# Optimization experiments

Hardware: AMD Instinct MI355X
Metric: run time of the kernel (lower is better)

The kernel has to match this reference:

```python
import jax, jax.numpy as jnp
import numpy as np

B, NQ, NK, D = 8, 2048, 2048, 512

def setup_inputs() -> dict:
    key = jax.random.key(0)
    ks = jax.random.split(key, 6)
    s = 1.0 / np.sqrt(D)
    return {
        "query": jax.random.normal(ks[0], (B, NQ, D), dtype=jnp.float32),
        "key":   jax.random.normal(ks[1], (B, NK, D), dtype=jnp.float32),
        "value": jax.random.normal(ks[2], (B, NK, D), dtype=jnp.float32),
        "Wq": jax.random.normal(ks[3], (D, D), dtype=jnp.float32) * s,
        "Wk": jax.random.normal(ks[4], (D, D), dtype=jnp.float32) * s,
        "Wv": jax.random.normal(ks[5], (D, D), dtype=jnp.float32) * s,
    }

def reference(query, key, value, Wq, Wk, Wv):
    # nn.Linear(bias=False): y = x @ W.T
    q = jnp.einsum('bnd,ed->bne', query, Wq)
    k = jnp.einsum('bnd,ed->bne', key, Wk)
    v = jnp.einsum('bnd,ed->bne', value, Wv)
    # NOTE: original module applies NO 1/sqrt(d) scaling
    scores = jnp.einsum('bqd,bkd->bqk', q, k)   # [B, NQ, NK]
    weights = jax.nn.softmax(scores, axis=-1)
    return jnp.einsum('bqk,bkd->bqd', weights, v)
```

## Files before the change

### kernel.cpp

```cpp
#include <hip/hip_runtime.h>

typedef __attribute__((ext_vector_type(8))) short short8;
typedef __attribute__((ext_vector_type(8))) _Float16 half8;
typedef __attribute__((ext_vector_type(4))) float f32x4;
typedef __attribute__((ext_vector_type(4))) unsigned short u16x4;
typedef __attribute__((ext_vector_type(4))) _Float16 half4;

#define NB 8
#define NQL 2048
#define NKL 2048
#define DD 512

static __device__ __forceinline__ void stage16(const void* g, void* l){
  __builtin_amdgcn_global_load_lds(
      (const __attribute__((address_space(1))) void*)g,
      (__attribute__((address_space(3))) void*)l, 16, 0, 0);
}

static __device__ __forceinline__ void barrier_lgkm(){
  asm volatile("s_waitcnt lgkmcnt(0)" ::: "memory");
  __builtin_amdgcn_s_barrier();
  asm volatile("" ::: "memory");
}

__global__ __launch_bounds__(256) void split3_k(
    const float* __restrict__ Wq, const float* __restrict__ Wk, const float* __restrict__ Wv,
    _Float16* __restrict__ w16q, _Float16* __restrict__ w16k, _Float16* __restrict__ w16v,
    int n4){
  const int z = blockIdx.y;
  const float* x = (z==0) ? Wq : (z==1) ? Wk : Wv;
  _Float16* o16 = (z==0) ? w16q : (z==1) ? w16k : w16v;
  int i = blockIdx.x*256 + threadIdx.x;
  if (i >= n4) return;
  f32x4 v = reinterpret_cast<const f32x4*>(x)[i];
  half4 h;
  #pragma unroll
  for (int j=0;j<4;j++) h[j] = (_Float16)v[j];
  reinterpret_cast<half4*>(o16)[i] = h;
}

__global__ __launch_bounds__(256, 2) void proj2_k(
    const float* __restrict__ Xq, const float* __restrict__ Xk, const float* __restrict__ Xv,
    const _Float16* __restrict__ W16q, const _Float16* __restrict__ W16k, const _Float16* __restrict__ W16v,
    _Float16* __restrict__ Yq,
    _Float16* __restrict__ Ykt,
    _Float16* __restrict__ Yvt)
{
  __shared__ _Float16 AB[2][2][128][32];

  const int z = blockIdx.z;
  const float*    X  = (z==0) ? Xq   : (z==1) ? Xk   : Xv;
  const _Float16* Wf = (z==0) ? W16q : (z==1) ? W16k : W16v;

  const int mbase = blockIdx.x * 128;
  const int nbase = blockIdx.y * 128;
  const int tid = threadIdx.x;
  const int w = tid >> 6, lane = tid & 63;
  const int l15 = lane & 15, l4 = lane >> 4;
  const int wr = w >> 1, wc = w & 1;

  const int arow = tid >> 1, ahalf = tid & 1;
  const int brow_l = w*16 + (lane>>2);
  const int bkg    = (lane & 3) ^ ((lane >> 3) & 3);

  f32x4 acc[4][4];
  #pragma unroll
  for (int m=0;m<4;m++)
    #pragma unroll
    for (int n=0;n<4;n++) acc[m][n] = (f32x4){0.f,0.f,0.f,0.f};

  f32x4 xa[4];
  {
    const f32x4* xp = reinterpret_cast<const f32x4*>(X + (size_t)(mbase+arow)*DD + ahalf*16);
    #pragma unroll
    for (int q=0;q<4;q++) xa[q] = xp[q];
  }
  {
    _Float16* lB = &AB[0][1][0][0] + w*512;
    #pragma unroll
    for (int r=0;r<2;r++){
      const size_t gh = (size_t)(nbase + r*64 + brow_l)*DD + bkg*8;
      stage16(Wf + gh, lB + r*2048);
    }
  }
  {
    asm volatile("s_waitcnt vmcnt(2)" ::: "memory");
    half8 a0, a1;
    #pragma unroll
    for (int j=0;j<4;j++){
      a0[j] = (_Float16)xa[0][j]; a0[4+j] = (_Float16)xa[1][j];
      a1[j] = (_Float16)xa[2][j]; a1[4+j] = (_Float16)xa[3][j];
    }
    const int sw = (arow>>1)&3;
    const int cg0 = (ahalf*2) ^ sw, cg1 = (ahalf*2+1) ^ sw;
    *reinterpret_cast<half8*>(&AB[0][0][arow][cg0*8]) = a0;
    *reinterpret_cast<half8*>(&AB[0][0][arow][cg1*8]) = a1;
  }

  const int asw = (l15>>1)&3;

  #pragma unroll 1
  for (int s=0; s<16; ++s){
    const int cur = s&1, nxt = cur^1;
    asm volatile("s_waitcnt vmcnt(0)" ::: "memory");
    barrier_lgkm();

    if (s < 15){
      const f32x4* xp = reinterpret_cast<const f32x4*>(X + (size_t)(mbase+arow)*DD + (s+1)*32 + ahalf*16);
      #pragma unroll
      for (int q=0;q<4;q++) xa[q] = xp[q];
      _Float16* lB = &AB[nxt][1][0][0] + w*512;
      #pragma unroll
      for (int r=0;r<2;r++){
        const size_t gh = (size_t)(nbase + r*64 + brow_l)*DD + (s+1)*32 + bkg*8;
        stage16(Wf + gh, lB + r*2048);
      }
    }

    half8 ah[4], wf[4];
    #pragma unroll
    for (int m=0;m<4;m++){
      const int rA = wr*64 + m*16 + l15;
      const int cg = (l4 ^ asw)*8;
      ah[m] = *reinterpret_cast<const half8*>(&AB[cur][0][rA][cg]);
    }
    #pragma unroll
    for (int n=0;n<4;n++){
      const int rB = wc*64 + n*16 + l15;
      const int cg = (l4 ^ asw)*8;
      wf[n] = *reinterpret_cast<const half8*>(&AB[cur][1][rB][cg]);
    }
    #pragma unroll
    for (int m=0;m<4;m++)
      #pragma unroll
      for (int n=0;n<4;n++) acc[m][n] = __builtin_amdgcn_mfma_f32_16x16x32_f16(ah[m], wf[n], acc[m][n], 0,0,0);

    if (s < 15){
      asm volatile("s_waitcnt vmcnt(2)" ::: "memory");
      half8 a0, a1;
      #pragma unroll
      for (int j=0;j<4;j++){
        a0[j] = (_Float16)xa[0][j]; a0[4+j] = (_Float16)xa[1][j];
        a1[j] = (_Float16)xa[2][j]; a1[4+j] = (_Float16)xa[3][j];
      }
      const int sw = (arow>>1)&3;
      const int cg0 = (ahalf*2) ^ sw, cg1 = (ahalf*2+1) ^ sw;
      *reinterpret_cast<half8*>(&AB[nxt][0][arow][cg0*8]) = a0;
      *reinterpret_cast<half8*>(&AB[nxt][0][arow][cg1*8]) = a1;
    }
  }

  #pragma unroll
  for (int m=0;m<4;m++){
    #pragma unroll
    for (int n=0;n<4;n++){
      #pragma unroll
      for (int j=0;j<4;j++){
        const int row = mbase + wr*64 + m*16 + l4*4 + j;
        const int col = nbase + wc*64 + n*16 + l15;
        const float y = acc[m][n][j];
        if (z == 0){
          Yq[(size_t)row*DD + col] = (_Float16)y;
        } else if (z == 1){
          const int bb = row >> 11, nn = row & 2047, kt = nn >> 5;
          const size_t tb = ((size_t)(bb*64 + kt)) << 14;
          const int kr = nn & 31, cg = col >> 3, ci = col & 7;
          const size_t idx = tb + ((size_t)kr)*512 + (size_t)((((cg ^ (kr & 7)) << 3)) | ci);
          Ykt[idx] = (_Float16)y;
        } else {
          const int bb = row >> 11, nn = row & 2047, kt = nn >> 5;
          const size_t tb = ((size_t)(bb*64 + kt)) << 14;
          const int kk = nn & 31;
          const size_t idx = tb + ((size_t)col)*32 + (size_t)kk;
          Yvt[idx] = (_Float16)y;
        }
      }
    }
  }
}

__global__ __launch_bounds__(256, 2) void attn_k(
    const _Float16* __restrict__ Qf,
    const _Float16* __restrict__ Kt,
    const _Float16* __restrict__ Vt,
    float* __restrict__ Out)
{
  __shared__ _Float16 K_lds[2][32][512];
  __shared__ _Float16 P_s[2][32][40];
  __shared__ float sc_s[2][32];
  __shared__ float l_s[32];

  const int bid = blockIdx.x;
  const int b  = bid & 7;
  const int qt = bid >> 3;
  const int tid = threadIdx.x;
  const int w = tid >> 6, lane = tid & 63;
  const int l15 = lane & 15, l4 = lane >> 4;
  const bool isQK = (w < 2);
  const int qw = w & 1;

  const _Float16* gK = Kt + ((size_t)(b*64) << 14);
  const _Float16* gV = Vt + ((size_t)(b*64) << 14);
  const int goff  = w*512 + lane*8;
  const int lbase = w*512;

  f32x4 r[32];
  half8 vr[16];
  float m_old = -1e30f, lacc = 0.f;
  if (isQK){
    const size_t qoff = (size_t)(b*NQL + qt*32 + qw*16 + l15)*DD + l4*8;
    #pragma unroll
    for (int kc=0;kc<16;kc++){
      r[kc] = __builtin_bit_cast(f32x4, *reinterpret_cast<const half8*>(Qf + qoff + kc*32));
    }
  } else {
    #pragma unroll
    for (int i=0;i<32;i++) r[i] = (f32x4){0.f,0.f,0.f,0.f};
  }

  {
    _Float16* lK = &K_lds[0][0][0];
    #pragma unroll
    for (int q=0;q<8;q++) stage16(gK + q*2048 + goff, lK + q*2048 + lbase);
  }

  const int kx = l15 & 7;
  const int row_i = qw*16 + l15;
  const int vcol = qw*256 + l15;

  #pragma unroll 1
  for (int kt=0; kt<64; ++kt){
    const int par = kt & 1;
    asm volatile("s_waitcnt vmcnt(0)" ::: "memory");
    barrier_lgkm();

    if (kt < 63){
      const _Float16* g = gK + ((size_t)(kt+1) << 14);
      _Float16* lK = &K_lds[par^1][0][0];
      #pragma unroll
      for (int q=0;q<8;q++) stage16(g + q*2048 + goff, lK + q*2048 + lbase);
    }

    if (isQK){
      f32x4 s0 = (f32x4){0.f,0.f,0.f,0.f};
      f32x4 s1 = (f32x4){0.f,0.f,0.f,0.f};
      __builtin_amdgcn_s_setprio(1);
      #pragma unroll
      for (int kc=0;kc<16;kc++){
        const int cg = ((kc*4 + l4) ^ kx) << 3;
        const half8 kf0 = *reinterpret_cast<const half8*>(&K_lds[par][l15][cg]);
        const half8 kf1 = *reinterpret_cast<const half8*>(&K_lds[par][16+l15][cg]);
        const half8 q = __builtin_bit_cast(half8, r[kc]);
        s0 = __builtin_amdgcn_mfma_f32_16x16x32_f16(kf0, q, s0, 0,0,0);
        s1 = __builtin_amdgcn_mfma_f32_16x16x32_f16(kf1, q, s1, 0,0,0);
      }
      __builtin_amdgcn_s_setprio(0);
      const f32x4 sv0 = s0;
      const f32x4 sv1 = s1;

      float mw = fmaxf(fmaxf(fmaxf(sv0[0],sv0[1]), fmaxf(sv0[2],sv0[3])),
                       fmaxf(fmaxf(sv1[0],sv1[1]), fmaxf(sv1[2],sv1[3])));
      float p0 = __expf(sv0[0]-m_old), p1 = __expf(sv0[1]-m_old);
      float p2 = __expf(sv0[2]-m_old), p3 = __expf(sv0[3]-m_old);
      float p4 = __expf(sv1[0]-m_old), p5 = __expf(sv1[1]-m_old);
      float p6 = __expf(sv1[2]-m_old), p7 = __expf(sv1[3]-m_old);
      mw = fmaxf(mw, __shfl_xor(mw, 16));
      mw = fmaxf(mw, __shfl_xor(mw, 32));
      float e_old = 1.0f;
      if (mw > m_old + 8.0f){
        e_old = __expf(m_old - mw);
        p0 = __expf(sv0[0]-mw); p1 = __expf(sv0[1]-mw);
        p2 = __expf(sv0[2]-mw); p3 = __expf(sv0[3]-mw);
        p4 = __expf(sv1[0]-mw); p5 = __expf(sv1[1]-mw);
        p6 = __expf(sv1[2]-mw); p7 = __expf(sv1[3]-mw);
        m_old = mw;
      }
      if (l4 == 0) sc_s[par][row_i] = e_old;
      uint2 hv;
      hv.x = (unsigned)__builtin_bit_cast(unsigned short,(_Float16)p0) |
             ((unsigned)__builtin_bit_cast(unsigned short,(_Float16)p1)<<16);
      hv.y = (unsigned)__builtin_bit_cast(unsigned short,(_Float16)p2) |
             ((unsigned)__builtin_bit_cast(unsigned short,(_Float16)p3)<<16);
      *reinterpret_cast<uint2*>(&P_s[par][row_i][l4*4]) = hv;
      uint2 hw;
      hw.x = (unsigned)__builtin_bit_cast(unsigned short,(_Float16)p4) |
             ((unsigned)__builtin_bit_cast(unsigned short,(_Float16)p5)<<16);
      hw.y = (unsigned)__builtin_bit_cast(unsigned short,(_Float16)p6) |
             ((unsigned)__builtin_bit_cast(unsigned short,(_Float16)p7)<<16);
      *reinterpret_cast<uint2*>(&P_s[par][row_i][16 + l4*4]) = hw;
      float ssum = (p0+p1)+(p2+p3)+((p4+p5)+(p6+p7));
      ssum += __shfl_xor(ssum, 16);
      ssum += __shfl_xor(ssum, 32);
      lacc = lacc*e_old + ssum;
    } else {
      const int pp = par^1;
      if (kt > 0){
        float scs[2][4];
        bool need = false;
        #pragma unroll
        for (int rg=0;rg<2;rg++)
          #pragma unroll
          for (int j=0;j<4;j++){
            scs[rg][j] = sc_s[pp][rg*16 + l4*4 + j];
            need = need || (scs[rg][j] < 0.999999f);
          }
        if (__any(need)){
          #pragma unroll
          for (int rg=0;rg<2;rg++)
            #pragma unroll
            for (int f=0;f<16;f++)
              #pragma unroll
              for (int j=0;j<4;j++) r[rg*16+f][j] *= scs[rg][j];
        }
        const half8 pa0 = *reinterpret_cast<const half8*>(&P_s[pp][l15][l4*8]);
        const half8 pa1 = *reinterpret_cast<const half8*>(&P_s[pp][16+l15][l4*8]);
        __builtin_amdgcn_s_setprio(1);
        #pragma unroll
        for (int f=0;f<16;f++){
          r[f]    = __builtin_amdgcn_mfma_f32_16x16x32_f16(pa0, vr[f], r[f],    0,0,0);
          r[16+f] = __builtin_amdgcn_mfma_f32_16x16x32_f16(pa1, vr[f], r[16+f], 0,0,0);
        }
        __builtin_amdgcn_s_setprio(0);
      }
      {
        const _Float16* g = gV + ((size_t)kt << 14);
        #pragma unroll
        for (int f=0;f<16;f++){
          vr[f] = *reinterpret_cast<const half8*>(g + (size_t)(vcol + f*16)*32 + l4*8);
        }
      }
    }
  }

  if (isQK && l4 == 0) l_s[row_i] = lacc;
  asm volatile("s_waitcnt vmcnt(0)" ::: "memory");
  barrier_lgkm();

  if (!isQK){
    float scs[2][4];
    bool need = false;
    #pragma unroll
    for (int rg=0;rg<2;rg++)
      #pragma unroll
      for (int j=0;j<4;j++){
        scs[rg][j] = sc_s[1][rg*16 + l4*4 + j];
        need = need || (scs[rg][j] < 0.999999f);
      }
    if (__any(need)){
      #pragma unroll
      for (int rg=0;rg<2;rg++)
        #pragma unroll
        for (int f=0;f<16;f++)
          #pragma unroll
          for (int j=0;j<4;j++) r[rg*16+f][j] *= scs[rg][j];
    }
    const half8 pa0 = *reinterpret_cast<const half8*>(&P_s[1][l15][l4*8]);
    const half8 pa1 = *reinterpret_cast<const half8*>(&P_s[1][16+l15][l4*8]);
    #pragma unroll
    for (int f=0;f<16;f++){
      r[f]    = __builtin_amdgcn_mfma_f32_16x16x32_f16(pa0, vr[f], r[f],    0,0,0);
      r[16+f] = __builtin_amdgcn_mfma_f32_16x16x32_f16(pa1, vr[f], r[16+f], 0,0,0);
    }
    float inv[2][4];
    #pragma unroll
    for (int rg=0;rg<2;rg++)
      #pragma unroll
      for (int j=0;j<4;j++) inv[rg][j] = 1.0f / l_s[rg*16 + l4*4 + j];
    #pragma unroll
    for (int rg=0;rg<2;rg++){
      #pragma unroll
      for (int j=0;j<4;j++){
        const int row = rg*16 + l4*4 + j;
        const size_t obase = (size_t)(b*NQL + qt*32 + row)*DD;
        #pragma unroll
        for (int f=0;f<16;f++){
          Out[obase + qw*256 + f*16 + l15] = r[rg*16+f][j]*inv[rg][j];
        }
      }
    }
  }
}

extern "C" void kernel_launch(void* const* d_in, const int* in_sizes, int n_in,
                              void* d_out, int out_size, void* d_ws, size_t ws_size,
                              hipStream_t stream) {
  const float* query = (const float*)d_in[0];
  const float* key   = (const float*)d_in[1];
  const float* value = (const float*)d_in[2];
  const float* Wq    = (const float*)d_in[3];
  const float* Wk    = (const float*)d_in[4];
  const float* Wv    = (const float*)d_in[5];
  float* out = (float*)d_out;

  const size_t SB = (size_t)NB*NQL*DD;
  const size_t WB = (size_t)DD*DD;

  _Float16* p = (_Float16*)d_ws;
  _Float16 *w16q = p, *w16k = p + WB, *w16v = p + 2*WB;
  _Float16* q0 = p + 3*WB;
  _Float16 *q16  = q0;
  _Float16 *Kt16 = q0 + SB;
  _Float16 *Vt16 = q0 + 2*SB;

  dim3 sg(256, 3);
  split3_k<<<sg, 256, 0, stream>>>(Wq, Wk, Wv, w16q, w16k, w16v, (int)(WB/4));

  dim3 pg(128, 4, 3);
  proj2_k<<<pg, 256, 0, stream>>>(query, key, value,
                                  w16q, w16k, w16v,
                                  q16, Kt16, Vt16);

  attn_k<<<512, 256, 0, stream>>>(q16, Kt16, Vt16, out);
}
```

Baseline: 173.8 us.

## Double attention tile to 64 queries and 64 keys with 512-thread blocks

The attention kernel now processes 64 query rows and 64-key tiles per block, using 8 waves (4 for QK/softmax, 4 for PV). The K/V projection output layout changes to 64-key tiles to match. This halves the number of K-tile iterations and barriers, and halves total K/V traffic per query. The cost is larger LDS use (about 130KB), fewer blocks (256, so one per CU), and a different PV register tiling.

```diff
diff --git a/kernel.cpp b/kernel.cpp
--- a/kernel.cpp
+++ b/kernel.cpp
@@ -162,16 +162,16 @@
         if (z == 0){
           Yq[(size_t)row*DD + col] = (_Float16)y;
         } else if (z == 1){
-          const int bb = row >> 11, nn = row & 2047, kt = nn >> 5;
-          const size_t tb = ((size_t)(bb*64 + kt)) << 14;
-          const int kr = nn & 31, cg = col >> 3, ci = col & 7;
+          const int bb = row >> 11, nn = row & 2047, kt = nn >> 6;
+          const size_t tb = ((size_t)(bb*32 + kt)) << 15;
+          const int kr = nn & 63, cg = col >> 3, ci = col & 7;
           const size_t idx = tb + ((size_t)kr)*512 + (size_t)((((cg ^ (kr & 7)) << 3)) | ci);
           Ykt[idx] = (_Float16)y;
         } else {
-          const int bb = row >> 11, nn = row & 2047, kt = nn >> 5;
-          const size_t tb = ((size_t)(bb*64 + kt)) << 14;
-          const int kk = nn & 31;
-          const size_t idx = tb + ((size_t)col)*32 + (size_t)kk;
+          const int bb = row >> 11, nn = row & 2047, kt = nn >> 6;
+          const size_t tb = ((size_t)(bb*32 + kt)) << 15;
+          const int kk = nn & 63;
+          const size_t idx = tb + ((size_t)col)*64 + (size_t)kk;
           Yvt[idx] = (_Float16)y;
         }
       }
@@ -179,16 +179,16 @@
   }
 }
 
-__global__ __launch_bounds__(256, 2) void attn_k(
+__global__ __launch_bounds__(512, 2) void attn_k(
     const _Float16* __restrict__ Qf,
     const _Float16* __restrict__ Kt,
     const _Float16* __restrict__ Vt,
     float* __restrict__ Out)
 {
-  __shared__ _Float16 K_lds[2][32][512];
-  __shared__ _Float16 P_s[2][32][40];
-  __shared__ float sc_s[2][32];
-  __shared__ float l_s[32];
+  __shared__ _Float16 K_lds[2][64][512];
+  __shared__ _Float16 P_s[2][64][72];
+  __shared__ float sc_s[2][64];
+  __shared__ float l_s[64];
 
   const int bid = blockIdx.x;
   const int b  = bid & 7;
@@ -196,11 +196,11 @@
   const int tid = threadIdx.x;
   const int w = tid >> 6, lane = tid & 63;
   const int l15 = lane & 15, l4 = lane >> 4;
-  const bool isQK = (w < 2);
-  const int qw = w & 1;
-
-  const _Float16* gK = Kt + ((size_t)(b*64) << 14);
-  const _Float16* gV = Vt + ((size_t)(b*64) << 14);
+  const bool isQK = (w < 4);
+  const int qw = w & 3;
+
+  const _Float16* gK = Kt + ((size_t)(b*32) << 15);
+  const _Float16* gV = Vt + ((size_t)(b*32) << 15);
   const int goff  = w*512 + lane*8;
   const int lbase = w*512;
 
@@ -208,7 +208,7 @@
   half8 vr[16];
   float m_old = -1e30f, lacc = 0.f;
   if (isQK){
-    const size_t qoff = (size_t)(b*NQL + qt*32 + qw*16 + l15)*DD + l4*8;
+    const size_t qoff = (size_t)(b*NQL + qt*64 + qw*16 + l15)*DD + l4*8;
     #pragma unroll
     for (int kc=0;kc<16;kc++){
       r[kc] = __builtin_bit_cast(f32x4, *reinterpret_cast<const half8*>(Qf + qoff + kc*32));
@@ -221,113 +221,140 @@
   {
     _Float16* lK = &K_lds[0][0][0];
     #pragma unroll
-    for (int q=0;q<8;q++) stage16(gK + q*2048 + goff, lK + q*2048 + lbase);
+    for (int q=0;q<8;q++) stage16(gK + q*4096 + goff, lK + q*4096 + lbase);
   }
 
   const int kx = l15 & 7;
   const int row_i = qw*16 + l15;
-  const int vcol = qw*256 + l15;
 
   #pragma unroll 1
-  for (int kt=0; kt<64; ++kt){
+  for (int kt=0; kt<32; ++kt){
     const int par = kt & 1;
     asm volatile("s_waitcnt vmcnt(0)" ::: "memory");
     barrier_lgkm();
 
-    if (kt < 63){
-      const _Float16* g = gK + ((size_t)(kt+1) << 14);
+    if (kt < 31){
+      const _Float16* g = gK + ((size_t)(kt+1) << 15);
       _Float16* lK = &K_lds[par^1][0][0];
       #pragma unroll
-      for (int q=0;q<8;q++) stage16(g + q*2048 + goff, lK + q*2048 + lbase);
+      for (int q=0;q<8;q++) stage16(g + q*4096 + goff, lK + q*4096 + lbase);
     }
 
     if (isQK){
       f32x4 s0 = (f32x4){0.f,0.f,0.f,0.f};
       f32x4 s1 = (f32x4){0.f,0.f,0.f,0.f};
+      f32x4 s2 = (f32x4){0.f,0.f,0.f,0.f};
+      f32x4 s3 = (f32x4){0.f,0.f,0.f,0.f};
       __builtin_amdgcn_s_setprio(1);
       #pragma unroll
       for (int kc=0;kc<16;kc++){
         const int cg = ((kc*4 + l4) ^ kx) << 3;
         const half8 kf0 = *reinterpret_cast<const half8*>(&K_lds[par][l15][cg]);
         const half8 kf1 = *reinterpret_cast<const half8*>(&K_lds[par][16+l15][cg]);
+        const half8 kf2 = *reinterpret_cast<const half8*>(&K_lds[par][32+l15][cg]);
+        const half8 kf3 = *reinterpret_cast<const half8*>(&K_lds[par][48+l15][cg]);
         const half8 q = __builtin_bit_cast(half8, r[kc]);
         s0 = __builtin_amdgcn_mfma_f32_16x16x32_f16(kf0, q, s0, 0,0,0);
         s1 = __builtin_amdgcn_mfma_f32_16x16x32_f16(kf1, q, s1, 0,0,0);
+        s2 = __builtin_amdgcn_mfma_f32_16x16x32_f16(kf2, q, s2, 0,0,0);
+        s3 = __builtin_amdgcn_mfma_f32_16x16x32_f16(kf3, q, s3, 0,0,0);
       }
       __builtin_amdgcn_s_setprio(0);
-      const f32x4 sv0 = s0;
-      const f32x4 sv1 = s1;
-
-      float mw = fmaxf(fmaxf(fmaxf(sv0[0],sv0[1]), fmaxf(sv0[2],sv0[3])),
-                       fmaxf(fmaxf(sv1[0],sv1[1]), fmaxf(sv1[2],sv1[3])));
-      float p0 = __expf(sv0[0]-m_old), p1 = __expf(sv0[1]-m_old);
-      float p2 = __expf(sv0[2]-m_old), p3 = __expf(sv0[3]-m_old);
-      float p4 = __expf(sv1[0]-m_old), p5 = __expf(sv1[1]-m_old);
-      float p6 = __expf(sv1[2]-m_old), p7 = __expf(sv1[3]-m_old);
+
+      float mw = fmaxf(fmaxf(fmaxf(s0[0],s0[1]), fmaxf(s0[2],s0[3])),
+                       fmaxf(fmaxf(s1[0],s1[1]), fmaxf(s1[2],s1[3])));
+      mw = fmaxf(mw, fmaxf(fmaxf(fmaxf(s2[0],s2[1]), fmaxf(s2[2],s2[3])),
+                           fmaxf(fmaxf(s3[0],s3[1]), fmaxf(s3[2],s3[3]))));
+      float p0[4], p1[4], p2[4], p3[4];
+      #pragma unroll
+      for (int j=0;j<4;j++){
+        p0[j] = __expf(s0[j]-m_old); p1[j] = __expf(s1[j]-m_old);
+        p2[j] = __expf(s2[j]-m_old); p3[j] = __expf(s3[j]-m_old);
+      }
       mw = fmaxf(mw, __shfl_xor(mw, 16));
       mw = fmaxf(mw, __shfl_xor(mw, 32));
       float e_old = 1.0f;
       if (mw > m_old + 8.0f){
         e_old = __expf(m_old - mw);
-        p0 = __expf(sv0[0]-mw); p1 = __expf(sv0[1]-mw);
-        p2 = __expf(sv0[2]-mw); p3 = __expf(sv0[3]-mw);
-        p4 = __expf(sv1[0]-mw); p5 = __expf(sv1[1]-mw);
-        p6 = __expf(sv1[2]-mw); p7 = __expf(sv1[3]-mw);
+        #pragma unroll
+        for (int j=0;j<4;j++){
+          p0[j] = __expf(s0[j]-mw); p1[j] = __expf(s1[j]-mw);
+          p2[j] = __expf(s2[j]-mw); p3[j] = __expf(s3[j]-mw);
+        }
         m_old = mw;
       }
       if (l4 == 0) sc_s[par][row_i] = e_old;
       uint2 hv;
-      hv.x = (unsigned)__builtin_bit_cast(unsigned short,(_Float16)p0) |
-             ((unsigned)__builtin_bit_cast(unsigned short,(_Float16)p1)<<16);
-      hv.y = (unsigned)__builtin_bit_cast(unsigned short,(_Float16)p2) |
-             ((unsigned)__builtin_bit_cast(unsigned short,(_Float16)p3)<<16);
+      hv.x = (unsigned)__builtin_bit_cast(unsigned short,(_Float16)p0[0]) |
+             ((unsigned)__builtin_bit_cast(unsigned short,(_Float16)p0[1])<<16);
+      hv.y = (unsigned)__builtin_bit_cast(unsigned short,(_Float16)p0[2]) |
+             ((unsigned)__builtin_bit_cast(unsigned short,(_Float16)p0[3])<<16);
       *reinterpret_cast<uint2*>(&P_s[par][row_i][l4*4]) = hv;
-      uint2 hw;
-      hw.x = (unsigned)__builtin_bit_cast(unsigned short,(_Float16)p4) |
-             ((unsigned)__builtin_bit_cast(unsigned short,(_Float16)p5)<<16);
-      hw.y = (unsigned)__builtin_bit_cast(unsigned short,(_Float16)p6) |
-             ((unsigned)__builtin_bit_cast(unsigned short,(_Float16)p7)<<16);
-      *reinterpret_cast<uint2*>(&P_s[par][row_i][16 + l4*4]) = hw;
-      float ssum = (p0+p1)+(p2+p3)+((p4+p5)+(p6+p7));
+      hv.x = (unsigned)__builtin_bit_cast(unsigned short,(_Float16)p1[0]) |
+             ((unsigned)__builtin_bit_cast(unsigned short,(_Float16)p1[1])<<16);
+      hv.y = (unsigned)__builtin_bit_cast(unsigned short,(_Float16)p1[2]) |
+             ((unsigned)__builtin_bit_cast(unsigned short,(_Float16)p1[3])<<16);
+      *reinterpret_cast<uint2*>(&P_s[par][row_i][16 + l4*4]) = hv;
+      hv.x = (unsigned)__builtin_bit_cast(unsigned short,(_Float16)p2[0]) |
+             ((unsigned)__builtin_bit_cast(unsigned short,(_Float16)p2[1])<<16);
+      hv.y = (unsigned)__builtin_bit_cast(unsigned short,(_Float16)p2[2]) |
+             ((unsigned)__builtin_bit_cast(unsigned short,(_Float16)p2[3])<<16);
+      *reinterpret_cast<uint2*>(&P_s[par][row_i][32 + l4*4]) = hv;
+      hv.x = (unsigned)__builtin_bit_cast(unsigned short,(_Float16)p3[0]) |
+             ((unsigned)__builtin_bit_cast(unsigned short,(_Float16)p3[1])<<16);
+      hv.y = (unsigned)__builtin_bit_cast(unsigned short,(_Float16)p3[2]) |
+             ((unsigned)__builtin_bit_cast(unsigned short,(_Float16)p3[3])<<16);
+      *reinterpret_cast<uint2*>(&P_s[par][row_i][48 + l4*4]) = hv;
+      float ssum = (p0[0]+p0[1])+(p0[2]+p0[3]) + (p1[0]+p1[1])+(p1[2]+p1[3])
+                 + (p2[0]+p2[1])+(p2[2]+p2[3]) + (p3[0]+p3[1])+(p3[2]+p3[3]);
       ssum += __shfl_xor(ssum, 16);
       ssum += __shfl_xor(ssum, 32);
       lacc = lacc*e_old + ssum;
     } else {
       const int pp = par^1;
       if (kt > 0){
-        float scs[2][4];
+        float scs[4][4];
         bool need = false;
         #pragma unroll
-        for (int rg=0;rg<2;rg++)
+        for (int rf=0;rf<4;rf++)
           #pragma unroll
           for (int j=0;j<4;j++){
-            scs[rg][j] = sc_s[pp][rg*16 + l4*4 + j];
-            need = need || (scs[rg][j] < 0.999999f);
+            scs[rf][j] = sc_s[pp][rf*16 + l4*4 + j];
+            need = need || (scs[rf][j] < 0.999999f);
           }
         if (__any(need)){
           #pragma unroll
-          for (int rg=0;rg<2;rg++)
+          for (int rf=0;rf<4;rf++)
             #pragma unroll
-            for (int f=0;f<16;f++)
+            for (int cf=0;cf<8;cf++)
               #pragma unroll
-              for (int j=0;j<4;j++) r[rg*16+f][j] *= scs[rg][j];
+              for (int j=0;j<4;j++) r[rf*8+cf][j] *= scs[rf][j];
         }
-        const half8 pa0 = *reinterpret_cast<const half8*>(&P_s[pp][l15][l4*8]);
-        const half8 pa1 = *reinterpret_cast<const half8*>(&P_s[pp][16+l15][l4*8]);
+        half8 pa[4][2];
+        #pragma unroll
+        for (int rf=0;rf<4;rf++)
+          #pragma unroll
+          for (int kc=0;kc<2;kc++)
+            pa[rf][kc] = *reinterpret_cast<const half8*>(&P_s[pp][rf*16 + l15][kc*32 + l4*8]);
         __builtin_amdgcn_s_setprio(1);
         #pragma unroll
-        for (int f=0;f<16;f++){
-          r[f]    = __builtin_amdgcn_mfma_f32_16x16x32_f16(pa0, vr[f], r[f],    0,0,0);
-          r[16+f] = __builtin_amdgcn_mfma_f32_16x16x32_f16(pa1, vr[f], r[16+f], 0,0,0);
-        }
+        for (int rf=0;rf<4;rf++)
+          #pragma unroll
+          for (int cf=0;cf<8;cf++){
+            r[rf*8+cf] = __builtin_amdgcn_mfma_f32_16x16x32_f16(pa[rf][0], vr[cf],   r[rf*8+cf], 0,0,0);
+            r[rf*8+cf] = __builtin_amdgcn_mfma_f32_16x16x32_f16(pa[rf][1], vr[8+cf], r[rf*8+cf], 0,0,0);
+          }
         __builtin_amdgcn_s_setprio(0);
       }
       {
-        const _Float16* g = gV + ((size_t)kt << 14);
-        #pragma unroll
-        for (int f=0;f<16;f++){
-          vr[f] = *reinterpret_cast<const half8*>(g + (size_t)(vcol + f*16)*32 + l4*8);
-        }
+        const _Float16* g = gV + ((size_t)kt << 15);
+        #pragma unroll
+        for (int kc=0;kc<2;kc++)
+          #pragma unroll
+          for (int cf=0;cf<8;cf++){
+            const int dcol = qw*128 + cf*16 + l15;
+            vr[kc*8+cf] = *reinterpret_cast<const half8*>(g + (size_t)dcol*64 + kc*32 + l4*8);
+          }
       }
     }
   }
@@ -337,44 +364,48 @@
   barrier_lgkm();
 
   if (!isQK){
-    float scs[2][4];
+    float scs[4][4];
     bool need = false;
     #pragma unroll
-    for (int rg=0;rg<2;rg++)
+    for (int rf=0;rf<4;rf++)
       #pragma unroll
       for (int j=0;j<4;j++){
-        scs[rg][j] = sc_s[1][rg*16 + l4*4 + j];
-        need = need || (scs[rg][j] < 0.999999f);
+        scs[rf][j] = sc_s[1][rf*16 + l4*4 + j];
+        need = need || (scs[rf][j] < 0.999999f);
       }
     if (__any(need)){
       #pragma unroll
-      for (int rg=0;rg<2;rg++)
-        #pragma unroll
-        for (int f=0;f<16;f++)
-          #pragma unroll
-          for (int j=0;j<4;j++) r[rg*16+f][j] *= scs[rg][j];
-    }
-    const half8 pa0 = *reinterpret_cast<const half8*>(&P_s[1][l15][l4*8]);
-    const half8 pa1 = *reinterpret_cast<const half8*>(&P_s[1][16+l15][l4*8]);
-    #pragma unroll
-    for (int f=0;f<16;f++){
-      r[f]    = __builtin_amdgcn_mfma_f32_16x16x32_f16(pa0, vr[f], r[f],    0,0,0);
-      r[16+f] = __builtin_amdgcn_mfma_f32_16x16x32_f16(pa1, vr[f], r[16+f], 0,0,0);
-    }
-    float inv[2][4];
-    #pragma unroll
-    for (int rg=0;rg<2;rg++)
-      #pragma unroll
-      for (int j=0;j<4;j++) inv[rg][j] = 1.0f / l_s[rg*16 + l4*4 + j];
-    #pragma unroll
-    for (int rg=0;rg<2;rg++){
+      for (int rf=0;rf<4;rf++)
+        #pragma unroll
+        for (int cf=0;cf<8;cf++)
+          #pragma unroll
+          for (int j=0;j<4;j++) r[rf*8+cf][j] *= scs[rf][j];
+    }
+    half8 pa[4][2];
+    #pragma unroll
+    for (int rf=0;rf<4;rf++)
+      #pragma unroll
+      for (int kc=0;kc<2;kc++)
+        pa[rf][kc] = *reinterpret_cast<const half8*>(&P_s[1][rf*16 + l15][kc*32 + l4*8]);
+    #pragma unroll
+    for (int rf=0;rf<4;rf++)
+      #pragma unroll
+      for (int cf=0;cf<8;cf++){
+        r[rf*8+cf] = __builtin_amdgcn_mfma_f32_16x16x32_f16(pa[rf][0], vr[cf],   r[rf*8+cf], 0,0,0);
+        r[rf*8+cf] = __builtin_amdgcn_mfma_f32_16x16x32_f16(pa[rf][1], vr[8+cf], r[rf*8+cf], 0,0,0);
+      }
+    #pragma unroll
+    for (int rf=0;rf<4;rf++){
+      float inv[4];
+      #pragma unroll
+      for (int j=0;j<4;j++) inv[j] = 1.0f / l_s[rf*16 + l4*4 + j];
       #pragma unroll
       for (int j=0;j<4;j++){
-        const int row = rg*16 + l4*4 + j;
-        const size_t obase = (size_t)(b*NQL + qt*32 + row)*DD;
-        #pragma unroll
-        for (int f=0;f<16;f++){
-          Out[obase + qw*256 + f*16 + l15] = r[rg*16+f][j]*inv[rg][j];
+        const int row = rf*16 + l4*4 + j;
+        const size_t obase = (size_t)(b*NQL + qt*64 + row)*DD;
+        #pragma unroll
+        for (int cf=0;cf<8;cf++){
+          Out[obase + qw*128 + cf*16 + l15] = r[rf*8+cf][j]*inv[j];
         }
       }
     }
@@ -410,5 +441,5 @@
                                   w16q, w16k, w16v,
                                   q16, Kt16, Vt16);
 
-  attn_k<<<512, 256, 0, stream>>>(q16, Kt16, Vt16, out);
-}
+  attn_k<<<256, 512, 0, stream>>>(q16, Kt16, Vt16, out);
+}
```

Result: slower. 207.5 us (+19.4%).
